# Optimization experiments

Hardware: AMD Instinct MI355X
Metric: run time of the kernel (lower is better)

## Reference

```python
import jax, jax.numpy as jnp
import numpy as np

NUM_HEADS = 8
NUM_POINTS = 4


def setup_inputs() -> dict:
    key = jax.random.key(0)
    ks = jax.random.split(key, 10)
    B, H, W, D = 8, 64, 64, 256
    N = H * W
    nh, P = NUM_HEADS, NUM_POINTS

    def xavier(k, shape):
        fan_in, fan_out = shape[0], shape[1]
        lim = float(np.sqrt(6.0 / (fan_in + fan_out)))
        return jax.random.uniform(k, shape, jnp.float32, -lim, lim)

    x = jax.random.normal(ks[0], (B, N, D), jnp.float32)
    qkv_w = xavier(ks[1], (D, 3 * D))
    qkv_b = jnp.zeros((3 * D,), jnp.float32)
    # offset network is zero-init in the module; use small random weights so the
    # deformable sampling is actually exercised (offsets nonzero).
    off_w = jax.random.normal(ks[2], (D, nh * P * 2), jnp.float32) * 0.01
    off_b = jnp.zeros((nh * P * 2,), jnp.float32)
    attw_w = xavier(ks[3], (D, nh * P))
    attw_b = jnp.zeros((nh * P,), jnp.float32)
    proj_w = xavier(ks[4], (D, D))
    proj_b = jnp.zeros((D,), jnp.float32)
    return {
        "x": x, "qkv_w": qkv_w, "qkv_b": qkv_b,
        "off_w": off_w, "off_b": off_b,
        "attw_w": attw_w, "attw_b": attw_b,
        "proj_w": proj_w, "proj_b": proj_b,
        "H": 64, "W": 64,
    }


def _deformable_forward(x, qkv_w, qkv_b, off_w, off_b, attw_w, attw_b, proj_w, proj_b, H, W):
    B, N, D = x.shape
    nh, P = NUM_HEADS, NUM_POINTS
    hd = D // nh

    qkv = x @ qkv_w + qkv_b                      # [B,N,3D] (q,k computed but unused, as in the original)
    v = qkv[..., 2 * D:].reshape(B, N, nh, hd)   # [B,N,nh,hd]

    offsets = jnp.tanh((x @ off_w + off_b).reshape(B, N, nh, P, 2)) * 2.0

    ys, xs = jnp.meshgrid(jnp.arange(H, dtype=x.dtype), jnp.arange(W, dtype=x.dtype), indexing="ij")
    ref = jnp.stack([xs, ys], axis=-1).reshape(N, 2)          # [N,2] (x,y) pixel coords
    loc = ref[None, :, None, None, :] + offsets               # [B,N,nh,P,2] pixel coords
    # (module normalizes to [-1,1] then grid_sample align_corners=True un-normalizes
    #  back to exactly these pixel coordinates, so we sample at `loc` directly)

    # value as flat spatial map per head: [B,nh,hd,N], n = y*W + x
    vf = v.transpose(0, 2, 3, 1).reshape(B, nh, hd, N)

    gx, gy = loc[..., 0], loc[..., 1]
    x0 = jnp.floor(gx); y0 = jnp.floor(gy)
    x1 = x0 + 1.0;      y1 = y0 + 1.0
    wx1 = gx - x0; wx0 = 1.0 - wx1
    wy1 = gy - y0; wy0 = 1.0 - wy1

    def corner(xi, yi, w):
        # bilinear corner with zeros padding: zero weight if corner out of bounds
        valid = (xi >= 0) & (xi < W) & (yi >= 0) & (yi < H)
        idx = (jnp.clip(yi, 0, H - 1) * W + jnp.clip(xi, 0, W - 1)).astype(jnp.int32)
        idx2 = idx.transpose(0, 2, 1, 3).reshape(B, nh, N * P)          # [B,nh,N*P]
        g = jnp.take_along_axis(vf, idx2[:, :, None, :], axis=3)        # [B,nh,hd,N*P]
        w2 = (w * valid.astype(x.dtype)).transpose(0, 2, 1, 3).reshape(B, nh, 1, N * P)
        return g * w2

    sampled = (corner(x0, y0, wx0 * wy0) + corner(x1, y0, wx1 * wy0)
               + corner(x0, y1, wx0 * wy1) + corner(x1, y1, wx1 * wy1))
    sampled = sampled.reshape(B, nh, hd, N, P)

    attn = jax.nn.softmax((x @ attw_w + attw_b).reshape(B, N, nh, P), axis=-1)
    out = jnp.einsum("bhcnp,bnhp->bnhc", sampled, attn).reshape(B, N, D)
    return out @ proj_w + proj_b


def reference(x, qkv_w, qkv_b, off_w, off_b, attw_w, attw_b, proj_w, proj_b, H, W):
    return _deformable_forward(x, qkv_w, qkv_b, off_w, off_b, attw_w, attw_b, proj_w, proj_b, H, W)
```

## Files before the change

### kernel.cpp

```cpp
#include <hip/hip_runtime.h>
#include <hip/hip_bf16.h>
#include <cmath>

#define NN 4096
typedef __attribute__((ext_vector_type(8))) short short8;
typedef __attribute__((ext_vector_type(4))) float f32x4;

__device__ __forceinline__ float bf2f(unsigned short u) {
  union { unsigned int i; float f; } c; c.i = ((unsigned int)u) << 16; return c.f;
}

__global__ __launch_bounds__(256) void cvt_w(
    const float* __restrict__ qkv_w, const float* __restrict__ off_w,
    const float* __restrict__ attw_w, const float* __restrict__ proj_w,
    __hip_bfloat16* __restrict__ wcatT, __hip_bfloat16* __restrict__ pjT)
{
  for (int i = blockIdx.x * 256 + threadIdx.x; i < 98304 + 65536; i += 65536) {
    if (i < 98304) {
      int c = i >> 8, k = i & 255;
      float v;
      if (c < 256)      v = qkv_w[k * 768 + 512 + c];
      else if (c < 320) v = off_w[k * 64 + (c - 256)];
      else if (c < 352) v = attw_w[k * 32 + (c - 320)];
      else              v = 0.f;
      wcatT[i] = __float2bfloat16(v);
    } else {
      int j = i - 98304; int c = j >> 8, k = j & 255;
      pjT[j] = __float2bfloat16(proj_w[k * 256 + c]);
    }
  }
}

__global__ __launch_bounds__(256) void gemm_voff(
    const float* __restrict__ x,
    const __hip_bfloat16* __restrict__ wcatT,
    const float* __restrict__ vbias,
    const float* __restrict__ off_b, const float* __restrict__ attw_b,
    __hip_bfloat16* __restrict__ vb,
    unsigned int* __restrict__ table)
{
  __shared__ float smemf[12800];
  short* As = (short*)smemf;
  short* Bs = As + 128 * 40;
  float (*L)[100] = (float(*)[100])smemf;

  const int t = threadIdx.x;
  const int m0 = blockIdx.y * 128, n0 = blockIdx.x * 128;
  const int wave = t >> 6, lane = t & 63, q = lane >> 4, ln = lane & 15;
  const int wm = (wave & 1) * 64, wn = (wave >> 1) * 64;

  f32x4 acc[4][4] = {};

  const int srow = t >> 1, skh = (t & 1) * 16;
  const float* apg = x + (size_t)(m0 + srow) * 256 + skh;
  const __hip_bfloat16* bpg = wcatT + (size_t)(n0 + srow) * 256 + skh;

  for (int k0 = 0; k0 < 256; k0 += 32) {
    float4 f0 = *(const float4*)(apg + k0);
    float4 f1 = *(const float4*)(apg + k0 + 4);
    float4 f2 = *(const float4*)(apg + k0 + 8);
    float4 f3 = *(const float4*)(apg + k0 + 12);
    alignas(16) __hip_bfloat16 cv[16] = {
      __float2bfloat16(f0.x), __float2bfloat16(f0.y), __float2bfloat16(f0.z), __float2bfloat16(f0.w),
      __float2bfloat16(f1.x), __float2bfloat16(f1.y), __float2bfloat16(f1.z), __float2bfloat16(f1.w),
      __float2bfloat16(f2.x), __float2bfloat16(f2.y), __float2bfloat16(f2.z), __float2bfloat16(f2.w),
      __float2bfloat16(f3.x), __float2bfloat16(f3.y), __float2bfloat16(f3.z), __float2bfloat16(f3.w)};
    *(int4*)&As[srow * 40 + skh]     = ((int4*)cv)[0];
    *(int4*)&As[srow * 40 + skh + 8] = ((int4*)cv)[1];
    *(int4*)&Bs[srow * 40 + skh]     = *(const int4*)(bpg + k0);
    *(int4*)&Bs[srow * 40 + skh + 8] = *(const int4*)(bpg + k0 + 8);
    __syncthreads();

    short8 a[4], b[4];
#pragma unroll
    for (int i = 0; i < 4; ++i) a[i] = *(const short8*)&As[(wm + i * 16 + ln) * 40 + q * 8];
#pragma unroll
    for (int j = 0; j < 4; ++j) b[j] = *(const short8*)&Bs[(wn + j * 16 + ln) * 40 + q * 8];
#pragma unroll
    for (int i = 0; i < 4; ++i)
#pragma unroll
      for (int j = 0; j < 4; ++j)
        acc[i][j] = __builtin_amdgcn_mfma_f32_16x16x32_bf16(a[i], b[j], acc[i][j], 0, 0, 0);
    __syncthreads();
  }

  if (n0 < 256) {
#pragma unroll
    for (int j = 0; j < 4; ++j) {
      int col = n0 + wn + j * 16 + ln;
      float bv = vbias[col];
#pragma unroll
      for (int i = 0; i < 4; ++i) {
        int rowb = m0 + wm + i * 16 + q * 4;
#pragma unroll
        for (int r = 0; r < 4; ++r)
          vb[(size_t)(rowb + r) * 256 + col] = __float2bfloat16(acc[i][j][r] + bv);
      }
    }
  } else {
#pragma unroll
    for (int j = 0; j < 4; ++j) {
      int col = wn + j * 16 + ln;
      if (col < 96) {
        float bv = (col < 64) ? off_b[col] : attw_b[col - 64];
#pragma unroll
        for (int i = 0; i < 4; ++i)
#pragma unroll
          for (int r = 0; r < 4; ++r)
            L[wm + i * 16 + q * 4 + r][col] = acc[i][j][r] + bv;
      }
    }
    __syncthreads();

#pragma unroll
    for (int it = 0; it < 4; ++it) {
      int pl = t + it * 256;
      int rr = pl >> 3, h = pl & 7;
      int row = m0 + rr;
      int nl = row & (NN - 1);
      float refx = (float)(nl & 63);
      float refy = (float)(nl >> 6);

      float a0 = L[rr][64 + h * 4 + 0], a1 = L[rr][64 + h * 4 + 1];
      float a2 = L[rr][64 + h * 4 + 2], a3 = L[rr][64 + h * 4 + 3];
      float mx = fmaxf(fmaxf(a0, a1), fmaxf(a2, a3));
      float e0 = expf(a0 - mx), e1 = expf(a1 - mx), e2 = expf(a2 - mx), e3 = expf(a3 - mx);
      float inv = 1.f / (e0 + e1 + e2 + e3);
      float at[4] = {e0 * inv, e1 * inv, e2 * inv, e3 * inv};

      alignas(16) unsigned short idxs[16];
      alignas(16) _Float16 wsv[16];
#pragma unroll
      for (int p = 0; p < 4; ++p) {
        float gx = refx + 2.f * tanhf(L[rr][h * 8 + p * 2 + 0]);
        float gy = refy + 2.f * tanhf(L[rr][h * 8 + p * 2 + 1]);
        float x0f = floorf(gx), y0f = floorf(gy);
        int x0 = (int)x0f, y0 = (int)y0f;
        int x1 = x0 + 1,   y1 = y0 + 1;
        float wx1 = gx - x0f, wx0 = 1.f - wx1;
        float wy1 = gy - y0f, wy0 = 1.f - wy1;
        int cx0 = min(max(x0, 0), 63), cx1 = min(max(x1, 0), 63);
        int cy0 = min(max(y0, 0), 63), cy1 = min(max(y1, 0), 63);
        float vx0 = (x0 >= 0) ? 1.f : 0.f;
        float vx1 = (x1 <= 63) ? 1.f : 0.f;
        float vy0 = (y0 >= 0) ? 1.f : 0.f;
        float vy1 = (y1 <= 63) ? 1.f : 0.f;
        vx0 *= (x0 <= 63) ? 1.f : 0.f;
        vx1 *= (x1 >= 0) ? 1.f : 0.f;
        vy0 *= (y0 <= 63) ? 1.f : 0.f;
        vy1 *= (y1 >= 0) ? 1.f : 0.f;
        float ap = at[p];
        idxs[p * 4 + 0] = (unsigned short)(cy0 * 64 + cx0);
        idxs[p * 4 + 1] = (unsigned short)(cy0 * 64 + cx1);
        idxs[p * 4 + 2] = (unsigned short)(cy1 * 64 + cx0);
        idxs[p * 4 + 3] = (unsigned short)(cy1 * 64 + cx1);
        wsv[p * 4 + 0] = (_Float16)(ap * wx0 * wy0 * vx0 * vy0);
        wsv[p * 4 + 1] = (_Float16)(ap * wx1 * wy0 * vx1 * vy0);
        wsv[p * 4 + 2] = (_Float16)(ap * wx0 * wy1 * vx0 * vy1);
        wsv[p * 4 + 3] = (_Float16)(ap * wx1 * wy1 * vx1 * vy1);
      }
      uint4* dst = (uint4*)(table + (size_t)(row * 8 + h) * 16);
      dst[0] = *(uint4*)&idxs[0];
      dst[1] = *(uint4*)&idxs[8];
      dst[2] = *(uint4*)&wsv[0];
      dst[3] = *(uint4*)&wsv[8];
    }
  }
}

__global__ __launch_bounds__(256) void sample_kernel(
    const __hip_bfloat16* __restrict__ v,
    const unsigned int* __restrict__ table,
    __hip_bfloat16* __restrict__ y)
{
  __shared__ uint4 Tab[256];
  const int t = threadIdx.x;
  const int p0 = blockIdx.x * 64;
  Tab[t] = *(const uint4*)(table + (size_t)p0 * 16 + t * 4);
  __syncthreads();

  const int g = t & 3, p = t >> 2;
  const int pg = p0 + p;
  const int h = pg & 7;
  const int row = pg >> 3;
  const int b = row >> 12;
  const unsigned short* ip = (const unsigned short*)&Tab[p * 4];
  const _Float16* wp = (const _Float16*)((const char*)&Tab[p * 4] + 32);
  const char* vbase = (const char*)(v + (size_t)b * NN * 256 + h * 32 + g * 8);

  float acc[8] = {};
#pragma unroll
  for (int j = 0; j < 16; ++j) {
    float w = (float)wp[j];
    int idx = ip[j];
    int4 pk = *(const int4*)(vbase + (size_t)idx * 512);
    const unsigned short* u = (const unsigned short*)&pk;
#pragma unroll
    for (int c = 0; c < 8; ++c) acc[c] += w * bf2f(u[c]);
  }
  alignas(16) __hip_bfloat16 o[8];
#pragma unroll
  for (int c = 0; c < 8; ++c) o[c] = __float2bfloat16(acc[c]);
  *(int4*)((char*)y + ((size_t)row * 256 + h * 32 + g * 8) * 2) = *(int4*)o;
}

__global__ __launch_bounds__(256) void gemm_proj(
    const short* __restrict__ A, const short* __restrict__ BT,
    const float* __restrict__ bias, float* __restrict__ out)
{
  __shared__ short As[128 * 40];
  __shared__ short Bs[128 * 40];
  const int t = threadIdx.x;
  const int m0 = blockIdx.y * 128, n0 = blockIdx.x * 128;
  const int wave = t >> 6, lane = t & 63, q = lane >> 4, ln = lane & 15;
  const int wm = (wave & 1) * 64, wn = (wave >> 1) * 64;

  f32x4 acc[4][4] = {};

  for (int k0 = 0; k0 < 256; k0 += 32) {
#pragma unroll
    for (int u = 0; u < 2; ++u) {
      int c = t + u * 256;
      int row = c >> 2, kq = c & 3;
      *(int4*)&As[row * 40 + kq * 8] =
          *(const int4*)&A[(size_t)(m0 + row) * 256 + k0 + kq * 8];
      *(int4*)&Bs[row * 40 + kq * 8] =
          *(const int4*)&BT[(size_t)(n0 + row) * 256 + k0 + kq * 8];
    }
    __syncthreads();
    short8 a[4], b[4];
#pragma unroll
    for (int i = 0; i < 4; ++i) a[i] = *(const short8*)&As[(wm + i * 16 + ln) * 40 + q * 8];
#pragma unroll
    for (int j = 0; j < 4; ++j) b[j] = *(const short8*)&Bs[(wn + j * 16 + ln) * 40 + q * 8];
#pragma unroll
    for (int i = 0; i < 4; ++i)
#pragma unroll
      for (int j = 0; j < 4; ++j)
        acc[i][j] = __builtin_amdgcn_mfma_f32_16x16x32_bf16(a[i], b[j], acc[i][j], 0, 0, 0);
    __syncthreads();
  }

#pragma unroll
  for (int j = 0; j < 4; ++j) {
    int col = n0 + wn + j * 16 + ln;
    float bv = bias[col];
#pragma unroll
    for (int i = 0; i < 4; ++i) {
      int rowb = m0 + wm + i * 16 + q * 4;
#pragma unroll
      for (int r = 0; r < 4; ++r)
        out[(size_t)(rowb + r) * 256 + col] = acc[i][j][r] + bv;
    }
  }
}

extern "C" void kernel_launch(void* const* d_in, const int* in_sizes, int n_in,
                              void* d_out, int out_size, void* d_ws, size_t ws_size,
                              hipStream_t stream) {
  const float* x      = (const float*)d_in[0];
  const float* qkv_w  = (const float*)d_in[1];
  const float* qkv_b  = (const float*)d_in[2];
  const float* off_w  = (const float*)d_in[3];
  const float* off_b  = (const float*)d_in[4];
  const float* attw_w = (const float*)d_in[5];
  const float* attw_b = (const float*)d_in[6];
  const float* proj_w = (const float*)d_in[7];
  const float* proj_b = (const float*)d_in[8];
  float* out = (float*)d_out;

  char* ws = (char*)d_ws;
  __hip_bfloat16* vb    = (__hip_bfloat16*)(ws);
  __hip_bfloat16* yb    = (__hip_bfloat16*)(ws + 16777216);
  unsigned int*   table = (unsigned int*)  (ws + 33554432);
  __hip_bfloat16* wcatT = (__hip_bfloat16*)(ws + 50331648);
  __hip_bfloat16* pjT   = (__hip_bfloat16*)(ws + 50528256);

  cvt_w<<<256, 256, 0, stream>>>(qkv_w, off_w, attw_w, proj_w, wcatT, pjT);

  dim3 g1(3, 256);
  gemm_voff<<<g1, 256, 0, stream>>>(x, wcatT, qkv_b + 512, off_b, attw_b, vb, table);

  sample_kernel<<<4096, 256, 0, stream>>>(vb, table, yb);

  dim3 g2(2, 256);
  gemm_proj<<<g2, 256, 0, stream>>>((const short*)yb, (const short*)pjT, proj_b, out);
}
```

Measured before the change: 160.7 us.

## Compute full 384-column V/offset GEMM per 128-row block with 512 threads

The value/offset GEMM now has each 512-thread block cover all 384 output columns for its 128 rows, instead of three 256-thread blocks per row tile. Each block converts x to bf16 once rather than three times, and the sampling-table epilogue runs in every block. The weight-conversion kernel is reorganised so each block handles one k row with column-per-thread reads from global memory. In exchange the grid has fewer blocks (256), each with more accumulators per wave, which can lower occupancy and latency hiding.

```diff
diff --git a/kernel.cpp b/kernel.cpp
--- a/kernel.cpp
+++ b/kernel.cpp
@@ -15,23 +15,24 @@
     const float* __restrict__ attw_w, const float* __restrict__ proj_w,
     __hip_bfloat16* __restrict__ wcatT, __hip_bfloat16* __restrict__ pjT)
 {
-  for (int i = blockIdx.x * 256 + threadIdx.x; i < 98304 + 65536; i += 65536) {
-    if (i < 98304) {
-      int c = i >> 8, k = i & 255;
-      float v;
-      if (c < 256)      v = qkv_w[k * 768 + 512 + c];
-      else if (c < 320) v = off_w[k * 64 + (c - 256)];
-      else if (c < 352) v = attw_w[k * 32 + (c - 320)];
-      else              v = 0.f;
-      wcatT[i] = __float2bfloat16(v);
-    } else {
-      int j = i - 98304; int c = j >> 8, k = j & 255;
-      pjT[j] = __float2bfloat16(proj_w[k * 256 + c]);
-    }
-  }
-}
-
-__global__ __launch_bounds__(256) void gemm_voff(
+  const int t = threadIdx.x;
+  if (blockIdx.x < 256) {
+    int k = blockIdx.x;
+    wcatT[t * 256 + k] = __float2bfloat16(qkv_w[k * 768 + 512 + t]);
+    if (t < 128) {
+      int c2 = 256 + t;
+      float v = 0.f;
+      if (c2 < 320)      v = off_w[k * 64 + (c2 - 256)];
+      else if (c2 < 352) v = attw_w[k * 32 + (c2 - 320)];
+      wcatT[c2 * 256 + k] = __float2bfloat16(v);
+    }
+  } else {
+    int k = blockIdx.x - 256;
+    pjT[t * 256 + k] = __float2bfloat16(proj_w[k * 256 + t]);
+  }
+}
+
+__global__ __launch_bounds__(512) void gemm_voff(
     const float* __restrict__ x,
     const __hip_bfloat16* __restrict__ wcatT,
     const float* __restrict__ vbias,
@@ -45,49 +46,47 @@
   float (*L)[100] = (float(*)[100])smemf;
 
   const int t = threadIdx.x;
-  const int m0 = blockIdx.y * 128, n0 = blockIdx.x * 128;
+  const int m0 = blockIdx.x * 128;
   const int wave = t >> 6, lane = t & 63, q = lane >> 4, ln = lane & 15;
-  const int wm = (wave & 1) * 64, wn = (wave >> 1) * 64;
-
-  f32x4 acc[4][4] = {};
-
-  const int srow = t >> 1, skh = (t & 1) * 16;
-  const float* apg = x + (size_t)(m0 + srow) * 256 + skh;
-  const __hip_bfloat16* bpg = wcatT + (size_t)(n0 + srow) * 256 + skh;
+  const int wm = (wave & 1) * 64, wn = (wave >> 1) * 96;
+
+  f32x4 acc[4][6] = {};
+
+  const int arow = t >> 2, aseg = t & 3;
+  const float* apg = x + (size_t)(m0 + arow) * 256 + aseg * 8;
 
   for (int k0 = 0; k0 < 256; k0 += 32) {
     float4 f0 = *(const float4*)(apg + k0);
     float4 f1 = *(const float4*)(apg + k0 + 4);
-    float4 f2 = *(const float4*)(apg + k0 + 8);
-    float4 f3 = *(const float4*)(apg + k0 + 12);
-    alignas(16) __hip_bfloat16 cv[16] = {
+    alignas(16) __hip_bfloat16 cv[8] = {
       __float2bfloat16(f0.x), __float2bfloat16(f0.y), __float2bfloat16(f0.z), __float2bfloat16(f0.w),
-      __float2bfloat16(f1.x), __float2bfloat16(f1.y), __float2bfloat16(f1.z), __float2bfloat16(f1.w),
-      __float2bfloat16(f2.x), __float2bfloat16(f2.y), __float2bfloat16(f2.z), __float2bfloat16(f2.w),
-      __float2bfloat16(f3.x), __float2bfloat16(f3.y), __float2bfloat16(f3.z), __float2bfloat16(f3.w)};
-    *(int4*)&As[srow * 40 + skh]     = ((int4*)cv)[0];
-    *(int4*)&As[srow * 40 + skh + 8] = ((int4*)cv)[1];
-    *(int4*)&Bs[srow * 40 + skh]     = *(const int4*)(bpg + k0);
-    *(int4*)&Bs[srow * 40 + skh + 8] = *(const int4*)(bpg + k0 + 8);
-    __syncthreads();
-
-    short8 a[4], b[4];
+      __float2bfloat16(f1.x), __float2bfloat16(f1.y), __float2bfloat16(f1.z), __float2bfloat16(f1.w)};
+    *(int4*)&As[arow * 40 + aseg * 8] = *(int4*)cv;
+#pragma unroll
+    for (int i = 0; i < 3; ++i) {
+      int u = t + i * 512;
+      int brow = u >> 2, bseg = u & 3;
+      *(int4*)&Bs[brow * 40 + bseg * 8] =
+          *(const int4*)&wcatT[(size_t)brow * 256 + k0 + bseg * 8];
+    }
+    __syncthreads();
+    short8 a[4], b[6];
 #pragma unroll
     for (int i = 0; i < 4; ++i) a[i] = *(const short8*)&As[(wm + i * 16 + ln) * 40 + q * 8];
 #pragma unroll
-    for (int j = 0; j < 4; ++j) b[j] = *(const short8*)&Bs[(wn + j * 16 + ln) * 40 + q * 8];
+    for (int j = 0; j < 6; ++j) b[j] = *(const short8*)&Bs[(wn + j * 16 + ln) * 40 + q * 8];
 #pragma unroll
     for (int i = 0; i < 4; ++i)
 #pragma unroll
-      for (int j = 0; j < 4; ++j)
+      for (int j = 0; j < 6; ++j)
         acc[i][j] = __builtin_amdgcn_mfma_f32_16x16x32_bf16(a[i], b[j], acc[i][j], 0, 0, 0);
     __syncthreads();
   }
 
-  if (n0 < 256) {
-#pragma unroll
-    for (int j = 0; j < 4; ++j) {
-      int col = n0 + wn + j * 16 + ln;
+#pragma unroll
+  for (int j = 0; j < 6; ++j) {
+    int col = wn + j * 16 + ln;
+    if (col < 256) {
       float bv = vbias[col];
 #pragma unroll
       for (int i = 0; i < 4; ++i) {
@@ -96,75 +95,66 @@
         for (int r = 0; r < 4; ++r)
           vb[(size_t)(rowb + r) * 256 + col] = __float2bfloat16(acc[i][j][r] + bv);
       }
-    }
-  } else {
-#pragma unroll
-    for (int j = 0; j < 4; ++j) {
-      int col = wn + j * 16 + ln;
-      if (col < 96) {
-        float bv = (col < 64) ? off_b[col] : attw_b[col - 64];
-#pragma unroll
-        for (int i = 0; i < 4; ++i)
-#pragma unroll
-          for (int r = 0; r < 4; ++r)
-            L[wm + i * 16 + q * 4 + r][col] = acc[i][j][r] + bv;
-      }
-    }
-    __syncthreads();
-
-#pragma unroll
-    for (int it = 0; it < 4; ++it) {
-      int pl = t + it * 256;
-      int rr = pl >> 3, h = pl & 7;
-      int row = m0 + rr;
-      int nl = row & (NN - 1);
-      float refx = (float)(nl & 63);
-      float refy = (float)(nl >> 6);
-
-      float a0 = L[rr][64 + h * 4 + 0], a1 = L[rr][64 + h * 4 + 1];
-      float a2 = L[rr][64 + h * 4 + 2], a3 = L[rr][64 + h * 4 + 3];
-      float mx = fmaxf(fmaxf(a0, a1), fmaxf(a2, a3));
-      float e0 = expf(a0 - mx), e1 = expf(a1 - mx), e2 = expf(a2 - mx), e3 = expf(a3 - mx);
-      float inv = 1.f / (e0 + e1 + e2 + e3);
-      float at[4] = {e0 * inv, e1 * inv, e2 * inv, e3 * inv};
-
-      alignas(16) unsigned short idxs[16];
-      alignas(16) _Float16 wsv[16];
-#pragma unroll
-      for (int p = 0; p < 4; ++p) {
-        float gx = refx + 2.f * tanhf(L[rr][h * 8 + p * 2 + 0]);
-        float gy = refy + 2.f * tanhf(L[rr][h * 8 + p * 2 + 1]);
-        float x0f = floorf(gx), y0f = floorf(gy);
-        int x0 = (int)x0f, y0 = (int)y0f;
-        int x1 = x0 + 1,   y1 = y0 + 1;
-        float wx1 = gx - x0f, wx0 = 1.f - wx1;
-        float wy1 = gy - y0f, wy0 = 1.f - wy1;
-        int cx0 = min(max(x0, 0), 63), cx1 = min(max(x1, 0), 63);
-        int cy0 = min(max(y0, 0), 63), cy1 = min(max(y1, 0), 63);
-        float vx0 = (x0 >= 0) ? 1.f : 0.f;
-        float vx1 = (x1 <= 63) ? 1.f : 0.f;
-        float vy0 = (y0 >= 0) ? 1.f : 0.f;
-        float vy1 = (y1 <= 63) ? 1.f : 0.f;
-        vx0 *= (x0 <= 63) ? 1.f : 0.f;
-        vx1 *= (x1 >= 0) ? 1.f : 0.f;
-        vy0 *= (y0 <= 63) ? 1.f : 0.f;
-        vy1 *= (y1 >= 0) ? 1.f : 0.f;
-        float ap = at[p];
-        idxs[p * 4 + 0] = (unsigned short)(cy0 * 64 + cx0);
-        idxs[p * 4 + 1] = (unsigned short)(cy0 * 64 + cx1);
-        idxs[p * 4 + 2] = (unsigned short)(cy1 * 64 + cx0);
-        idxs[p * 4 + 3] = (unsigned short)(cy1 * 64 + cx1);
-        wsv[p * 4 + 0] = (_Float16)(ap * wx0 * wy0 * vx0 * vy0);
-        wsv[p * 4 + 1] = (_Float16)(ap * wx1 * wy0 * vx1 * vy0);
-        wsv[p * 4 + 2] = (_Float16)(ap * wx0 * wy1 * vx0 * vy1);
-        wsv[p * 4 + 3] = (_Float16)(ap * wx1 * wy1 * vx1 * vy1);
-      }
-      uint4* dst = (uint4*)(table + (size_t)(row * 8 + h) * 16);
-      dst[0] = *(uint4*)&idxs[0];
-      dst[1] = *(uint4*)&idxs[8];
-      dst[2] = *(uint4*)&wsv[0];
-      dst[3] = *(uint4*)&wsv[8];
-    }
+    } else if (col < 352) {
+      int lc = col - 256;
+      float bv = (lc < 64) ? off_b[lc] : attw_b[lc - 64];
+#pragma unroll
+      for (int i = 0; i < 4; ++i)
+#pragma unroll
+        for (int r = 0; r < 4; ++r)
+          L[wm + i * 16 + q * 4 + r][lc] = acc[i][j][r] + bv;
+    }
+  }
+  __syncthreads();
+
+#pragma unroll
+  for (int it = 0; it < 2; ++it) {
+    int pl = t + it * 512;
+    int rr = pl >> 3, h = pl & 7;
+    int row = m0 + rr;
+    int nl = row & (NN - 1);
+    float refx = (float)(nl & 63);
+    float refy = (float)(nl >> 6);
+
+    float a0 = L[rr][64 + h * 4 + 0], a1 = L[rr][64 + h * 4 + 1];
+    float a2 = L[rr][64 + h * 4 + 2], a3 = L[rr][64 + h * 4 + 3];
+    float mx = fmaxf(fmaxf(a0, a1), fmaxf(a2, a3));
+    float e0 = expf(a0 - mx), e1 = expf(a1 - mx), e2 = expf(a2 - mx), e3 = expf(a3 - mx);
+    float inv = 1.f / (e0 + e1 + e2 + e3);
+    float at[4] = {e0 * inv, e1 * inv, e2 * inv, e3 * inv};
+
+    alignas(16) unsigned short idxs[16];
+    alignas(16) _Float16 wsv[16];
+#pragma unroll
+    for (int p = 0; p < 4; ++p) {
+      float gx = refx + 2.f * tanhf(L[rr][h * 8 + p * 2 + 0]);
+      float gy = refy + 2.f * tanhf(L[rr][h * 8 + p * 2 + 1]);
+      float x0f = floorf(gx), y0f = floorf(gy);
+      int x0 = (int)x0f, y0 = (int)y0f;
+      int x1 = x0 + 1,   y1 = y0 + 1;
+      float wx1 = gx - x0f, wx0 = 1.f - wx1;
+      float wy1 = gy - y0f, wy0 = 1.f - wy1;
+      int cx0 = min(max(x0, 0), 63), cx1 = min(max(x1, 0), 63);
+      int cy0 = min(max(y0, 0), 63), cy1 = min(max(y1, 0), 63);
+      float vx0 = (x0 >= 0 && x0 <= 63) ? 1.f : 0.f;
+      float vx1 = (x1 >= 0 && x1 <= 63) ? 1.f : 0.f;
+      float vy0 = (y0 >= 0 && y0 <= 63) ? 1.f : 0.f;
+      float vy1 = (y1 >= 0 && y1 <= 63) ? 1.f : 0.f;
+      float ap = at[p];
+      idxs[p * 4 + 0] = (unsigned short)(cy0 * 64 + cx0);
+      idxs[p * 4 + 1] = (unsigned short)(cy0 * 64 + cx1);
+      idxs[p * 4 + 2] = (unsigned short)(cy1 * 64 + cx0);
+      idxs[p * 4 + 3] = (unsigned short)(cy1 * 64 + cx1);
+      wsv[p * 4 + 0] = (_Float16)(ap * wx0 * wy0 * vx0 * vy0);
+      wsv[p * 4 + 1] = (_Float16)(ap * wx1 * wy0 * vx1 * vy0);
+      wsv[p * 4 + 2] = (_Float16)(ap * wx0 * wy1 * vx0 * vy1);
+      wsv[p * 4 + 3] = (_Float16)(ap * wx1 * wy1 * vx1 * vy1);
+    }
+    uint4* dst = (uint4*)(table + ((size_t)row * 8 + h) * 16);
+    dst[0] = *(uint4*)&idxs[0];
+    dst[1] = *(uint4*)&idxs[8];
+    dst[2] = *(uint4*)&wsv[0];
+    dst[3] = *(uint4*)&wsv[8];
   }
 }
 
@@ -276,13 +266,9 @@
   __hip_bfloat16* wcatT = (__hip_bfloat16*)(ws + 50331648);
   __hip_bfloat16* pjT   = (__hip_bfloat16*)(ws + 50528256);
 
-  cvt_w<<<256, 256, 0, stream>>>(qkv_w, off_w, attw_w, proj_w, wcatT, pjT);
-
-  dim3 g1(3, 256);
-  gemm_voff<<<g1, 256, 0, stream>>>(x, wcatT, qkv_b + 512, off_b, attw_b, vb, table);
-
+  cvt_w<<<512, 256, 0, stream>>>(qkv_w, off_w, attw_w, proj_w, wcatT, pjT);
+  gemm_voff<<<256, 512, 0, stream>>>(x, wcatT, qkv_b + 512, off_b, attw_b, vb, table);
   sample_kernel<<<4096, 256, 0, stream>>>(vb, table, yb);
-
   dim3 g2(2, 256);
   gemm_proj<<<g2, 256, 0, stream>>>((const short*)yb, (const short*)pjT, proj_b, out);
 }
```

New measurement: 152.6 us. 1.05x faster.
